# Optimization experiments

Hardware: AMD Instinct MI355X
Metric: run time of the kernel (lower is better)

## Reference

```python
import jax, jax.numpy as jnp
from jax import lax
import numpy as np

N, W, H, C = 32, 64, 64, 256
D_STYLE = 256


def setup_inputs() -> dict:
    key = jax.random.key(0)
    k1, k2, k3, k4 = jax.random.split(key, 4)
    inputs = jax.random.normal(k1, (N, W, H, C), dtype=jnp.float32)
    style_coding = jax.random.normal(k2, (N, D_STYLE), dtype=jnp.float32)
    # he_normal-ish init scaling for the learned weights
    w_dense = jax.random.normal(k3, (D_STYLE, C), dtype=jnp.float32) * np.sqrt(2.0 / D_STYLE)
    w_conv = jax.random.normal(k4, (1, 1, C, C), dtype=jnp.float32) * np.sqrt(2.0 / C)
    return {"inputs": inputs, "style_coding": style_coding, "w_dense": w_dense, "w_conv": w_conv}


def reference(inputs, style_coding, w_dense, w_conv):
    # inputs: [N,W,H,C] (NHWC), style_coding: [N,D_style]
    c = inputs.shape[-1]
    scale = 1.0 / jnp.sqrt(jnp.float32(c))
    # Dense(fout_dim, use_bias=False, activation=LeakyReLU())  (keras default alpha=0.3)
    q = jax.nn.leaky_relu(style_coding @ w_dense, negative_slope=0.3)  # [N,C]
    # channel-wise attention: einsum('nwhc,nwhc->nc') with q broadcast over w,h
    ca_logits = jnp.einsum('nwhc,nc->nc', inputs, q) * scale           # [N,C]
    ca = jax.nn.softmax(ca_logits, axis=-1)[:, None, None, :]          # [N,1,1,C]
    # position-wise attention: einsum('nwhc,nwhc->nwh'), softmax over flattened W*H
    pa_logits = jnp.einsum('nwhc,nc->nwh', inputs, q) * scale          # [N,W,H]
    n, w, h = pa_logits.shape
    pa = jax.nn.softmax(pa_logits.reshape(n, w * h), axis=1).reshape(n, w, h, 1)
    x = inputs * ca * pa                                               # [N,W,H,C]
    # DarknetConv2D_BN_Leaky with no norm kwarg: 1x1 conv (no bias) + LeakyReLU(0.1)
    y = lax.conv_general_dilated(x, w_conv, window_strides=(1, 1), padding='SAME',
                                 dimension_numbers=('NHWC', 'HWIO', 'NHWC'))
    return jax.nn.leaky_relu(y, negative_slope=0.1)
```

## Files before the change

### kernel.cpp

```cpp
#include <hip/hip_runtime.h>


#define NBATCH 32
#define PIX 4096
#define CH 256
#define SCALE 0.0625f

typedef __attribute__((ext_vector_type(8))) short short8;
typedef __attribute__((ext_vector_type(4))) short short4v;
typedef __attribute__((ext_vector_type(4))) float floatx4;

__device__ __forceinline__ short f2bf(float x) {
    unsigned u = __builtin_bit_cast(unsigned, x);
    u += 0x7fffu + ((u >> 16) & 1u);
    return (short)(u >> 16);
}

__device__ __forceinline__ void gll16(const void* g, void* l) {
    __builtin_amdgcn_global_load_lds(
        (const __attribute__((address_space(1))) unsigned int*)g,
        (__attribute__((address_space(3))) unsigned int*)l, 16, 0, 0);
}

__global__ __launch_bounds__(256) void reduce_cast_q(
    const float* __restrict__ inp, const float* __restrict__ style,
    const float* __restrict__ wd,
    float* __restrict__ q_out, float* __restrict__ colsum_part,
    float* __restrict__ pa_logits, short* __restrict__ bf16in)
{
    __shared__ float s[256];
    __shared__ float q_s[256];
    const int n = blockIdx.y, chunk = blockIdx.x, t = threadIdx.x;

    s[t] = style[n * 256 + t];
    __syncthreads();
    float acc = 0.f;
#pragma unroll 8
    for (int k = 0; k < 256; ++k) acc += s[k] * wd[k * 256 + t];
    acc = acc > 0.f ? acc : 0.3f * acc;
    q_s[t] = acc;
    if (chunk == 0) q_out[n * 256 + t] = acc;
    __syncthreads();

    const int lane = t & 63, w = t >> 6;
    const float4 qv = *(const float4*)&q_s[lane * 4];
    float4 cs = make_float4(0.f, 0.f, 0.f, 0.f);
    const int pbase = chunk * 128 + w * 32;
    const float* base = inp + ((size_t)n * PIX + pbase) * CH;
    short* obase = bf16in + ((size_t)n * PIX + pbase) * CH;
#pragma unroll 4
    for (int j = 0; j < 32; ++j) {
        float4 v = *(const float4*)&base[(size_t)j * CH + lane * 4];
        float d = v.x * qv.x + v.y * qv.y + v.z * qv.z + v.w * qv.w;
        cs.x += v.x; cs.y += v.y; cs.z += v.z; cs.w += v.w;
        short4v sv;
        sv.x = f2bf(v.x); sv.y = f2bf(v.y); sv.z = f2bf(v.z); sv.w = f2bf(v.w);
        *(short4v*)&obase[(size_t)j * CH + lane * 4] = sv;
#pragma unroll
        for (int off = 32; off; off >>= 1) d += __shfl_xor(d, off);
        if (lane == 0) pa_logits[n * PIX + pbase + j] = d * SCALE;
    }
    *(float4*)&colsum_part[((size_t)n * 128 + chunk * 4 + w) * 256 + lane * 4] = cs;
}

__global__ __launch_bounds__(256) void softmax_wscale(
    const float* __restrict__ colsum_part, const float* __restrict__ q,
    const float* __restrict__ pa_logits, const float* __restrict__ wc,
    float* __restrict__ pa, short* __restrict__ wscaled)
{
    __shared__ float red[256];
    __shared__ float ca_s[256];
    __shared__ float wt[32][257];
    const int n = blockIdx.x, t = threadIdx.x;

    float csum = 0.f;
#pragma unroll 8
    for (int i = 0; i < 128; ++i) csum += colsum_part[((size_t)n * 128 + i) * 256 + t];
    float lg = csum * q[n * 256 + t] * SCALE;
    red[t] = lg; __syncthreads();
    for (int s = 128; s > 0; s >>= 1) {
        if (t < s) red[t] = fmaxf(red[t], red[t + s]);
        __syncthreads();
    }
    float m = red[0]; __syncthreads();
    float e = expf(lg - m);
    red[t] = e; __syncthreads();
    for (int s = 128; s > 0; s >>= 1) {
        if (t < s) red[t] += red[t + s];
        __syncthreads();
    }
    ca_s[t] = e / red[0];
    __syncthreads();

    float lv[16];
    float lmax = -1e30f;
#pragma unroll
    for (int i = 0; i < 16; ++i) {
        lv[i] = pa_logits[n * PIX + t + 256 * i];
        lmax = fmaxf(lmax, lv[i]);
    }
    red[t] = lmax; __syncthreads();
    for (int s = 128; s > 0; s >>= 1) {
        if (t < s) red[t] = fmaxf(red[t], red[t + s]);
        __syncthreads();
    }
    float M = red[0]; __syncthreads();
    float ev[16], lsum = 0.f;
#pragma unroll
    for (int i = 0; i < 16; ++i) { ev[i] = expf(lv[i] - M); lsum += ev[i]; }
    red[t] = lsum; __syncthreads();
    for (int s = 128; s > 0; s >>= 1) {
        if (t < s) red[t] += red[t + s];
        __syncthreads();
    }
    float inv = 1.0f / red[0];
#pragma unroll
    for (int i = 0; i < 16; ++i) pa[n * PIX + t + 256 * i] = ev[i] * inv;

    const int tx = t & 31, ty = t >> 5;
    for (int strip = 0; strip < 8; ++strip) {
        const int ci0 = strip * 32;
        __syncthreads();
#pragma unroll
        for (int r = 0; r < 4; ++r) {
            const int ci = ty + r * 8;
#pragma unroll
            for (int cb = 0; cb < 8; ++cb)
                wt[ci][cb * 32 + tx] = wc[(ci0 + ci) * 256 + cb * 32 + tx];
        }
        __syncthreads();
        const float cav = ca_s[ci0 + tx];
#pragma unroll
        for (int r = 0; r < 4; ++r) {
#pragma unroll
            for (int cb = 0; cb < 8; ++cb) {
                const int co = cb * 32 + ty + r * 8;
                wscaled[(size_t)n * 65536 + co * 256 + ci0 + tx] =
                    f2bf(wt[tx][co] * cav);
            }
        }
    }
}

__global__ __launch_bounds__(256, 2) void conv_mfma(
    const short* __restrict__ bf16in, const short* __restrict__ wscaled,
    const float* __restrict__ pa, float* __restrict__ out)
{
    __shared__ __attribute__((aligned(16))) short As[2][64 * 64];
    __shared__ __attribute__((aligned(16))) short Bs[2][256 * 64];

    const int n  = blockIdx.y;
    const int m0 = blockIdx.x * 64;
    const int tid = threadIdx.x;
    const int lane = tid & 63, wid = tid >> 6;
    const int l16 = lane & 15, quad = lane >> 4;
    const int l8r = lane >> 3, slot = lane & 7;

    floatx4 acc[4][4] = {};

    const short* Agb = bf16in + ((size_t)n * PIX + m0) * CH;
    const short* Bgb = wscaled + (size_t)n * 65536;

    auto stage = [&](int kb, int buf) {
        const int k0 = kb * 64;
#pragma unroll
        for (int i = 0; i < 2; ++i) {
            const int r = wid * 16 + i * 8 + l8r;
            gll16(Agb + (size_t)r * CH + k0 + ((slot ^ (r & 7)) << 3),
                  &As[buf][(wid * 16 + i * 8) * 64]);
        }
#pragma unroll
        for (int i = 0; i < 8; ++i) {
            const int c = wid * 64 + i * 8 + l8r;
            gll16(Bgb + (size_t)c * CH + k0 + ((slot ^ (c & 7)) << 3),
                  &Bs[buf][(wid * 64 + i * 8) * 64]);
        }
    };

    stage(0, 0);
    __syncthreads();

    for (int kb = 0; kb < 4; ++kb) {
        const int cur = kb & 1;
        if (kb < 3) stage(kb + 1, cur ^ 1);
#pragma unroll
        for (int kk2 = 0; kk2 < 2; ++kk2) {
            const int sx = ((kk2 * 4 + quad) ^ (l16 & 7)) << 3;
            short8 af[4], bfr[4];
#pragma unroll
            for (int mt = 0; mt < 4; ++mt)
                af[mt] = *(const short8*)&As[cur][(mt * 16 + l16) * 64 + sx];
#pragma unroll
            for (int nt = 0; nt < 4; ++nt)
                bfr[nt] = *(const short8*)&Bs[cur][(wid * 64 + nt * 16 + l16) * 64 + sx];
#pragma unroll
            for (int mt = 0; mt < 4; ++mt)
#pragma unroll
                for (int nt = 0; nt < 4; ++nt)
                    acc[mt][nt] = __builtin_amdgcn_mfma_f32_16x16x32_bf16(
                        af[mt], bfr[nt], acc[mt][nt], 0, 0, 0);
        }
        __syncthreads();
    }

#pragma unroll
    for (int mt = 0; mt < 4; ++mt) {
#pragma unroll
        for (int reg = 0; reg < 4; ++reg) {
            const int pix = m0 + mt * 16 + quad * 4 + reg;
            const float pav = pa[n * PIX + pix];
            float* orow = out + ((size_t)(n * PIX + pix)) * CH + wid * 64;
#pragma unroll
            for (int nt = 0; nt < 4; ++nt) {
                float z = acc[mt][nt][reg] * pav;
                orow[nt * 16 + l16] = z > 0.f ? z : 0.1f * z;
            }
        }
    }
}

extern "C" void kernel_launch(void* const* d_in, const int* in_sizes, int n_in,
                              void* d_out, int out_size, void* d_ws, size_t ws_size,
                              hipStream_t stream) {
    const float* inputs = (const float*)d_in[0];
    const float* style  = (const float*)d_in[1];
    const float* wdense = (const float*)d_in[2];
    const float* wconv  = (const float*)d_in[3];
    float* out = (float*)d_out;

    char* ws = (char*)d_ws;
    float* q           = (float*)(ws + 0);
    float* pa_logits   = (float*)(ws + 32768);
    float* pa          = (float*)(ws + 557056);
    float* colsum_part = (float*)(ws + 1081344);
    short* wscaled     = (short*)(ws + 5275648);
    short* bf16in      = (short*)(ws + 9469952);

    reduce_cast_q<<<dim3(32, NBATCH), 256, 0, stream>>>(inputs, style, wdense, q,
                                                        colsum_part, pa_logits, bf16in);
    softmax_wscale<<<NBATCH, 256, 0, stream>>>(colsum_part, q, pa_logits, wconv,
                                               pa, wscaled);
    conv_mfma<<<dim3(64, NBATCH), 256, 0, stream>>>(bf16in, wscaled, pa, out);
}
```

Baseline: 316.3 us.

## Split style GEMV, defer dot reductions via LDS, widen softmax, halve conv K-tile

The q GEMV moves into its own small kernel, so the 1024 reduce blocks no longer each recompute the 256x256 product. The reduce kernel buffers per-pixel partial dot products in LDS and reduces them once after the loop, replacing a six-step shuffle reduction on every pixel. The softmax/weight-scaling kernel runs 1024 threads per batch and uses wave shuffles instead of tree reductions with many barriers. The conv kernel uses K-tiles of 32 with a 4-way swizzle, halving LDS so four blocks fit per CU, at the cost of twice as many barrier-separated k-steps.

New measurement: 311.5 us. No clear change (-1.5%).

```diff
diff --git a/kernel.cpp b/kernel.cpp
--- a/kernel.cpp
+++ b/kernel.cpp
@@ -22,28 +22,29 @@
         (__attribute__((address_space(3))) unsigned int*)l, 16, 0, 0);
 }
 
-__global__ __launch_bounds__(256) void reduce_cast_q(
-    const float* __restrict__ inp, const float* __restrict__ style,
-    const float* __restrict__ wd,
-    float* __restrict__ q_out, float* __restrict__ colsum_part,
-    float* __restrict__ pa_logits, short* __restrict__ bf16in)
+__global__ __launch_bounds__(256) void style_kernel(
+    const float* __restrict__ style, const float* __restrict__ wd,
+    float* __restrict__ q)
 {
     __shared__ float s[256];
-    __shared__ float q_s[256];
-    const int n = blockIdx.y, chunk = blockIdx.x, t = threadIdx.x;
-
+    const int n = blockIdx.x, t = threadIdx.x;
     s[t] = style[n * 256 + t];
     __syncthreads();
     float acc = 0.f;
 #pragma unroll 8
     for (int k = 0; k < 256; ++k) acc += s[k] * wd[k * 256 + t];
-    acc = acc > 0.f ? acc : 0.3f * acc;
-    q_s[t] = acc;
-    if (chunk == 0) q_out[n * 256 + t] = acc;
-    __syncthreads();
-
-    const int lane = t & 63, w = t >> 6;
-    const float4 qv = *(const float4*)&q_s[lane * 4];
+    q[n * 256 + t] = acc > 0.f ? acc : 0.3f * acc;
+}
+
+__global__ __launch_bounds__(256) void reduce_cast(
+    const float* __restrict__ inp, const float* __restrict__ q,
+    float* __restrict__ colsum_part, float* __restrict__ pa_logits,
+    short* __restrict__ bf16in)
+{
+    __shared__ float part[4][32][67];
+    const int n = blockIdx.y, chunk = blockIdx.x;
+    const int t = threadIdx.x, lane = t & 63, w = t >> 6;
+    const float4 qv = *(const float4*)&q[n * 256 + lane * 4];
     float4 cs = make_float4(0.f, 0.f, 0.f, 0.f);
     const int pbase = chunk * 128 + w * 32;
     const float* base = inp + ((size_t)n * PIX + pbase) * CH;
@@ -51,110 +52,132 @@
 #pragma unroll 4
     for (int j = 0; j < 32; ++j) {
         float4 v = *(const float4*)&base[(size_t)j * CH + lane * 4];
-        float d = v.x * qv.x + v.y * qv.y + v.z * qv.z + v.w * qv.w;
         cs.x += v.x; cs.y += v.y; cs.z += v.z; cs.w += v.w;
+        part[w][j][lane] = v.x * qv.x + v.y * qv.y + v.z * qv.z + v.w * qv.w;
         short4v sv;
         sv.x = f2bf(v.x); sv.y = f2bf(v.y); sv.z = f2bf(v.z); sv.w = f2bf(v.w);
         *(short4v*)&obase[(size_t)j * CH + lane * 4] = sv;
-#pragma unroll
-        for (int off = 32; off; off >>= 1) d += __shfl_xor(d, off);
-        if (lane == 0) pa_logits[n * PIX + pbase + j] = d * SCALE;
-    }
+    }
+    __syncthreads();
+    const int p = lane & 31, seg = lane >> 5;
+    float s0 = 0.f, s1 = 0.f, s2 = 0.f, s3 = 0.f;
+#pragma unroll
+    for (int i = 0; i < 8; ++i) {
+        s0 += part[w][p][seg * 32 + i * 4 + 0];
+        s1 += part[w][p][seg * 32 + i * 4 + 1];
+        s2 += part[w][p][seg * 32 + i * 4 + 2];
+        s3 += part[w][p][seg * 32 + i * 4 + 3];
+    }
+    float sum = (s0 + s1) + (s2 + s3);
+    sum += __shfl_xor(sum, 32);
+    if (lane < 32) pa_logits[n * PIX + pbase + lane] = sum * SCALE;
     *(float4*)&colsum_part[((size_t)n * 128 + chunk * 4 + w) * 256 + lane * 4] = cs;
 }
 
-__global__ __launch_bounds__(256) void softmax_wscale(
+__global__ __launch_bounds__(1024) void softmax_wscale(
     const float* __restrict__ colsum_part, const float* __restrict__ q,
     const float* __restrict__ pa_logits, const float* __restrict__ wc,
     float* __restrict__ pa, short* __restrict__ wscaled)
 {
-    __shared__ float red[256];
+    __shared__ float red4[4][256];
+    __shared__ float wred[16];
     __shared__ float ca_s[256];
     __shared__ float wt[32][257];
     const int n = blockIdx.x, t = threadIdx.x;
-
-    float csum = 0.f;
+    const int lane = t & 63, wave = t >> 6;
+
+    {
+        const int ch = t & 255, seg = t >> 8;
+        float c0 = 0.f;
 #pragma unroll 8
-    for (int i = 0; i < 128; ++i) csum += colsum_part[((size_t)n * 128 + i) * 256 + t];
-    float lg = csum * q[n * 256 + t] * SCALE;
-    red[t] = lg; __syncthreads();
-    for (int s = 128; s > 0; s >>= 1) {
-        if (t < s) red[t] = fmaxf(red[t], red[t + s]);
-        __syncthreads();
-    }
-    float m = red[0]; __syncthreads();
-    float e = expf(lg - m);
-    red[t] = e; __syncthreads();
-    for (int s = 128; s > 0; s >>= 1) {
-        if (t < s) red[t] += red[t + s];
-        __syncthreads();
-    }
-    ca_s[t] = e / red[0];
-    __syncthreads();
-
-    float lv[16];
-    float lmax = -1e30f;
-#pragma unroll
-    for (int i = 0; i < 16; ++i) {
-        lv[i] = pa_logits[n * PIX + t + 256 * i];
+        for (int i = 0; i < 32; ++i)
+            c0 += colsum_part[((size_t)n * 128 + seg * 32 + i) * 256 + ch];
+        red4[seg][ch] = c0;
+    }
+    __syncthreads();
+
+    float lg = -1e30f, e = 0.f;
+    if (t < 256) {
+        float csum = red4[0][t] + red4[1][t] + red4[2][t] + red4[3][t];
+        lg = csum * q[n * 256 + t] * SCALE;
+    }
+    float m = lg;
+#pragma unroll
+    for (int off = 32; off; off >>= 1) m = fmaxf(m, __shfl_xor(m, off));
+    if (lane == 0) wred[wave] = m;
+    __syncthreads();
+    m = fmaxf(fmaxf(wred[0], wred[1]), fmaxf(wred[2], wred[3]));
+    if (t < 256) e = expf(lg - m);
+    float es = e;
+#pragma unroll
+    for (int off = 32; off; off >>= 1) es += __shfl_xor(es, off);
+    __syncthreads();
+    if (lane == 0) wred[wave] = es;
+    __syncthreads();
+    float S = wred[0] + wred[1] + wred[2] + wred[3];
+    if (t < 256) ca_s[t] = e / S;
+
+    float lv[4], lmax = -1e30f;
+#pragma unroll
+    for (int i = 0; i < 4; ++i) {
+        lv[i] = pa_logits[n * PIX + t + 1024 * i];
         lmax = fmaxf(lmax, lv[i]);
     }
-    red[t] = lmax; __syncthreads();
-    for (int s = 128; s > 0; s >>= 1) {
-        if (t < s) red[t] = fmaxf(red[t], red[t + s]);
-        __syncthreads();
-    }
-    float M = red[0]; __syncthreads();
-    float ev[16], lsum = 0.f;
-#pragma unroll
-    for (int i = 0; i < 16; ++i) { ev[i] = expf(lv[i] - M); lsum += ev[i]; }
-    red[t] = lsum; __syncthreads();
-    for (int s = 128; s > 0; s >>= 1) {
-        if (t < s) red[t] += red[t + s];
-        __syncthreads();
-    }
-    float inv = 1.0f / red[0];
-#pragma unroll
-    for (int i = 0; i < 16; ++i) pa[n * PIX + t + 256 * i] = ev[i] * inv;
-
-    const int tx = t & 31, ty = t >> 5;
+#pragma unroll
+    for (int off = 32; off; off >>= 1) lmax = fmaxf(lmax, __shfl_xor(lmax, off));
+    __syncthreads();
+    if (lane == 0) wred[wave] = lmax;
+    __syncthreads();
+    float M = wred[0];
+#pragma unroll
+    for (int i = 1; i < 16; ++i) M = fmaxf(M, wred[i]);
+    float ev[4], lsum = 0.f;
+#pragma unroll
+    for (int i = 0; i < 4; ++i) { ev[i] = expf(lv[i] - M); lsum += ev[i]; }
+#pragma unroll
+    for (int off = 32; off; off >>= 1) lsum += __shfl_xor(lsum, off);
+    __syncthreads();
+    if (lane == 0) wred[wave] = lsum;
+    __syncthreads();
+    float Ssum = 0.f;
+#pragma unroll
+    for (int i = 0; i < 16; ++i) Ssum += wred[i];
+    float inv = 1.0f / Ssum;
+#pragma unroll
+    for (int i = 0; i < 4; ++i) pa[n * PIX + t + 1024 * i] = ev[i] * inv;
+
+    const int tx = t & 31;
     for (int strip = 0; strip < 8; ++strip) {
         const int ci0 = strip * 32;
         __syncthreads();
 #pragma unroll
-        for (int r = 0; r < 4; ++r) {
-            const int ci = ty + r * 8;
-#pragma unroll
-            for (int cb = 0; cb < 8; ++cb)
-                wt[ci][cb * 32 + tx] = wc[(ci0 + ci) * 256 + cb * 32 + tx];
+        for (int r = 0; r < 8; ++r) {
+            const int idx = t + 1024 * r;
+            wt[idx >> 8][idx & 255] = wc[(ci0 + (idx >> 8)) * 256 + (idx & 255)];
         }
         __syncthreads();
         const float cav = ca_s[ci0 + tx];
 #pragma unroll
-        for (int r = 0; r < 4; ++r) {
-#pragma unroll
-            for (int cb = 0; cb < 8; ++cb) {
-                const int co = cb * 32 + ty + r * 8;
-                wscaled[(size_t)n * 65536 + co * 256 + ci0 + tx] =
-                    f2bf(wt[tx][co] * cav);
-            }
-        }
-    }
-}
-
-__global__ __launch_bounds__(256, 2) void conv_mfma(
+        for (int r = 0; r < 8; ++r) {
+            const int co = r * 32 + (t >> 5);
+            wscaled[(size_t)n * 65536 + co * 256 + ci0 + tx] = f2bf(wt[tx][co] * cav);
+        }
+    }
+}
+
+__global__ __launch_bounds__(256, 4) void conv_mfma(
     const short* __restrict__ bf16in, const short* __restrict__ wscaled,
     const float* __restrict__ pa, float* __restrict__ out)
 {
-    __shared__ __attribute__((aligned(16))) short As[2][64 * 64];
-    __shared__ __attribute__((aligned(16))) short Bs[2][256 * 64];
+    __shared__ __attribute__((aligned(16))) short As[2][64 * 32];
+    __shared__ __attribute__((aligned(16))) short Bs[2][256 * 32];
 
     const int n  = blockIdx.y;
     const int m0 = blockIdx.x * 64;
     const int tid = threadIdx.x;
     const int lane = tid & 63, wid = tid >> 6;
     const int l16 = lane & 15, quad = lane >> 4;
-    const int l8r = lane >> 3, slot = lane & 7;
+    const int r4 = lane >> 2, s4 = lane & 3;
 
     floatx4 acc[4][4] = {};
 
@@ -162,44 +185,43 @@
     const short* Bgb = wscaled + (size_t)n * 65536;
 
     auto stage = [&](int kb, int buf) {
-        const int k0 = kb * 64;
-#pragma unroll
-        for (int i = 0; i < 2; ++i) {
-            const int r = wid * 16 + i * 8 + l8r;
-            gll16(Agb + (size_t)r * CH + k0 + ((slot ^ (r & 7)) << 3),
-                  &As[buf][(wid * 16 + i * 8) * 64]);
-        }
-#pragma unroll
-        for (int i = 0; i < 8; ++i) {
-            const int c = wid * 64 + i * 8 + l8r;
-            gll16(Bgb + (size_t)c * CH + k0 + ((slot ^ (c & 7)) << 3),
-                  &Bs[buf][(wid * 64 + i * 8) * 64]);
+        const int k0 = kb * 32;
+        {
+            const int r = wid * 16 + r4;
+            gll16(Agb + (size_t)r * CH + k0 + ((s4 ^ ((r >> 1) & 3)) << 3),
+                  &As[buf][(wid * 16) * 32]);
+        }
+#pragma unroll
+        for (int i = 0; i < 4; ++i) {
+            const int c = wid * 64 + i * 16 + r4;
+            gll16(Bgb + (size_t)c * CH + k0 + ((s4 ^ ((c >> 1) & 3)) << 3),
+                  &Bs[buf][(wid * 64 + i * 16) * 32]);
         }
     };
 
     stage(0, 0);
     __syncthreads();
 
-    for (int kb = 0; kb < 4; ++kb) {
+    for (int kb = 0; kb < 8; ++kb) {
         const int cur = kb & 1;
-        if (kb < 3) stage(kb + 1, cur ^ 1);
-#pragma unroll
-        for (int kk2 = 0; kk2 < 2; ++kk2) {
-            const int sx = ((kk2 * 4 + quad) ^ (l16 & 7)) << 3;
-            short8 af[4], bfr[4];
-#pragma unroll
-            for (int mt = 0; mt < 4; ++mt)
-                af[mt] = *(const short8*)&As[cur][(mt * 16 + l16) * 64 + sx];
+        if (kb < 7) stage(kb + 1, cur ^ 1);
+        short8 af[4], bfr[4];
+#pragma unroll
+        for (int mt = 0; mt < 4; ++mt) {
+            const int row = mt * 16 + l16;
+            af[mt] = *(const short8*)&As[cur][row * 32 + ((quad ^ ((row >> 1) & 3)) << 3)];
+        }
+#pragma unroll
+        for (int nt = 0; nt < 4; ++nt) {
+            const int row = wid * 64 + nt * 16 + l16;
+            bfr[nt] = *(const short8*)&Bs[cur][row * 32 + ((quad ^ ((row >> 1) & 3)) << 3)];
+        }
+#pragma unroll
+        for (int mt = 0; mt < 4; ++mt)
 #pragma unroll
             for (int nt = 0; nt < 4; ++nt)
-                bfr[nt] = *(const short8*)&Bs[cur][(wid * 64 + nt * 16 + l16) * 64 + sx];
-#pragma unroll
-            for (int mt = 0; mt < 4; ++mt)
-#pragma unroll
-                for (int nt = 0; nt < 4; ++nt)
-                    acc[mt][nt] = __builtin_amdgcn_mfma_f32_16x16x32_bf16(
-                        af[mt], bfr[nt], acc[mt][nt], 0, 0, 0);
-        }
+                acc[mt][nt] = __builtin_amdgcn_mfma_f32_16x16x32_bf16(
+                    af[mt], bfr[nt], acc[mt][nt], 0, 0, 0);
         __syncthreads();
     }
 
@@ -236,9 +258,10 @@
     short* wscaled     = (short*)(ws + 5275648);
     short* bf16in      = (short*)(ws + 9469952);
 
-    reduce_cast_q<<<dim3(32, NBATCH), 256, 0, stream>>>(inputs, style, wdense, q,
-                                                        colsum_part, pa_logits, bf16in);
-    softmax_wscale<<<NBATCH, 256, 0, stream>>>(colsum_part, q, pa_logits, wconv,
-                                               pa, wscaled);
+    style_kernel<<<NBATCH, 256, 0, stream>>>(style, wdense, q);
+    reduce_cast<<<dim3(32, NBATCH), 256, 0, stream>>>(inputs, q, colsum_part,
+                                                      pa_logits, bf16in);
+    softmax_wscale<<<NBATCH, 1024, 0, stream>>>(colsum_part, q, pa_logits, wconv,
+                                                pa, wscaled);
     conv_mfma<<<dim3(64, NBATCH), 256, 0, stream>>>(bf16in, wscaled, pa, out);
 }
```
